# Kernel optimization log

Hardware: AMD Instinct MI355X
Metric: run time of the kernel (lower is better)

## Reference

```python
import jax, jax.numpy as jnp
import numpy as np

B, L, D, H, K = 4, 4096, 1024, 16, 256

def setup_inputs() -> dict:
    key = jax.random.key(0)
    ks = jax.random.split(key, 11)
    s = 0.02
    return {
        "x": jax.random.normal(ks[0], (B, L, D), jnp.float32),
        "Wq": jax.random.normal(ks[1], (D, D), jnp.float32) * s,
        "bq": jax.random.normal(ks[2], (D,), jnp.float32) * s,
        "Wk": jax.random.normal(ks[3], (D, D), jnp.float32) * s,
        "bk": jax.random.normal(ks[4], (D,), jnp.float32) * s,
        "Wv": jax.random.normal(ks[5], (D, D), jnp.float32) * s,
        "bv": jax.random.normal(ks[6], (D,), jnp.float32) * s,
        "E": jax.random.normal(ks[7], (L, K), jnp.float32),
        "F": jax.random.normal(ks[8], (L, K), jnp.float32),
        "Wo": jax.random.normal(ks[9], (D, D), jnp.float32) * s,
        "bo": jax.random.normal(ks[10], (D,), jnp.float32) * s,
        "n_heads": H,
    }

def reference(x, Wq, bq, Wk, bk, Wv, bv, E, F, Wo, bo, n_heads):
    Bc, Lc, Dc = x.shape
    hd = Dc // n_heads
    scale = hd ** -0.5
    # QKV projections (torch Linear: x @ W.T + b; here W stored as [in,out])
    q = (x @ Wq + bq).reshape(Bc, Lc, n_heads, hd)  # blhd
    k = (x @ Wk + bk).reshape(Bc, Lc, n_heads, hd)
    v = (x @ Wv + bv).reshape(Bc, Lc, n_heads, hd)
    # Low-rank projection of K/V sequence dim: L -> K
    kE = jnp.einsum('blhd,lk->bhkd', k, E[:Lc])
    vF = jnp.einsum('blhd,lk->bhkd', v, F[:Lc])
    # Attention over compressed dim k
    qk = jnp.einsum('blhd,bhkd->bhlk', q, kE) * scale
    attn = jax.nn.softmax(qk, axis=-1)
    out = jnp.einsum('bhlk,bhkd->blhd', attn, vF).reshape(Bc, Lc, Dc)
    return out @ Wo + bo
```

## Files before the change

kernel.cpp:

```cpp
#include <hip/hip_runtime.h>

typedef _Float16 half_t;
typedef __attribute__((ext_vector_type(8))) _Float16 f16x8;
typedef __attribute__((ext_vector_type(4))) _Float16 f16x4;
typedef __attribute__((ext_vector_type(4))) float f32x4;
typedef __attribute__((ext_vector_type(4))) float float4v;

__device__ __forceinline__ void gload_lds16(const void* g, void* l) {
  __builtin_amdgcn_global_load_lds(
      (const __attribute__((address_space(1))) void*)g,
      (__attribute__((address_space(3))) void*)l, 16, 0, 0);
}

template<int OUTMODE>
__global__ __launch_bounds__(512, 2)
void gemm_big(const half_t* __restrict__ A, const half_t* __restrict__ Bt,
              void* __restrict__ Cv, const float* __restrict__ bias, float alpha)
{
  __shared__ __attribute__((aligned(16))) char lds[131072];
  const int tid = threadIdx.x, w = tid >> 6, lane = tid & 63;
  const int wr = w >> 2, wc = w & 3;
  const int g = lane >> 4, cc = lane & 15;
  const int m0 = blockIdx.x * 256, n0 = blockIdx.y * 256;

  const int srow2 = tid >> 2, sslot = tid & 3;
  const int swslot = sslot ^ ((srow2 >> 1) & 3);
  const int swr = (g ^ ((cc >> 1) & 3)) << 4;

  const f32x4 zero = {0.f, 0.f, 0.f, 0.f};
  f32x4 acc[8][4];
#pragma unroll
  for (int i = 0; i < 8; ++i)
#pragma unroll
    for (int j = 0; j < 4; ++j) acc[i][j] = zero;

  auto STAGE_HALF = [&](int ktile, int hh, char* sb) {
    const int kk = hh >> 1, isB = hh & 1;
    const half_t* src = isB ? Bt : A;
    const int base_row = isB ? n0 : m0;
    const long rowoff = (long)(base_row + srow2) * 1024 + ktile * 64 + kk * 32 + swslot * 8;
    char* d = sb + isB * 32768 + kk * 16384;
    gload_lds16(src + rowoff,          d + tid * 16);
    gload_lds16(src + rowoff + 131072, d + 8192 + tid * 16);
  };

  {
    char* b0 = lds;
    STAGE_HALF(0, 0, b0); STAGE_HALF(0, 1, b0);
    STAGE_HALF(0, 2, b0); STAGE_HALF(0, 3, b0);
  }
  asm volatile("s_waitcnt vmcnt(4)" ::: "memory");
  __builtin_amdgcn_s_barrier();

#pragma unroll 1
  for (int n = 0; n < 16; ++n) {
    const char* rb = lds + ((n & 1) << 16);
    char* sb = lds + (((n + 1) & 1) << 16);
    f16x8 bf[4];
#pragma unroll
    for (int ph = 0; ph < 4; ++ph) {
      const int kk = ph >> 1, fh = ph & 1;
      f16x8 af[4];
      const char* Ah = rb + kk * 16384;
#pragma unroll
      for (int mf = 0; mf < 4; ++mf)
        af[mf] = *(const f16x8*)(Ah + (wr * 128 + fh * 64 + mf * 16 + cc) * 64 + swr);
      if (fh == 0) {
        const char* Bh = rb + 32768 + kk * 16384;
#pragma unroll
        for (int nf = 0; nf < 4; ++nf)
          bf[nf] = *(const f16x8*)(Bh + (wc * 64 + nf * 16 + cc) * 64 + swr);
      }
      if (n < 15) STAGE_HALF(n + 1, ph, sb);
      __builtin_amdgcn_sched_barrier(0);
      __builtin_amdgcn_s_barrier();
      asm volatile("s_waitcnt lgkmcnt(0)" ::: "memory");
      __builtin_amdgcn_sched_barrier(0);
      __builtin_amdgcn_s_setprio(1);
#pragma unroll
      for (int mf = 0; mf < 4; ++mf)
#pragma unroll
        for (int nf = 0; nf < 4; ++nf)
          acc[fh * 4 + mf][nf] =
              __builtin_amdgcn_mfma_f32_16x16x32_f16(af[mf], bf[nf], acc[fh * 4 + mf][nf], 0, 0, 0);
      __builtin_amdgcn_s_setprio(0);
      __builtin_amdgcn_sched_barrier(0);
      if (ph == 1) {
        if (n < 15) { asm volatile("s_waitcnt vmcnt(4)" ::: "memory"); }
        else        { asm volatile("s_waitcnt vmcnt(0)" ::: "memory"); }
      } else if (ph == 3) {
        if (n < 15) { asm volatile("s_waitcnt vmcnt(4)" ::: "memory"); }
      }
      __builtin_amdgcn_s_barrier();
    }
  }

#pragma unroll
  for (int mf = 0; mf < 8; ++mf)
#pragma unroll
    for (int nf = 0; nf < 4; ++nf)
#pragma unroll
      for (int r = 0; r < 4; ++r) {
        const int row = m0 + wr * 128 + mf * 16 + g * 4 + r;
        const int col = n0 + wc * 64 + nf * 16 + cc;
        float v = (acc[mf][nf][r] + bias[col]) * alpha;
        if (OUTMODE == 0) {
          ((float*)Cv)[(long)row * 1024 + col] = v;
        } else {
          const int bb = row >> 12, l = row & 4095, h = col >> 6, d = col & 63;
          ((half_t*)Cv)[(((long)(bb * 16 + h) * 4096 + l) << 6) + d] = (half_t)v;
        }
      }
}

template<int SK>
__global__ __launch_bounds__(256, 2)
void gemm_xef(const half_t* __restrict__ A, const half_t* __restrict__ Bt,
              float* __restrict__ Cv, int lda, int ldb, long sB, long sC)
{
  __shared__ __attribute__((aligned(16))) half_t As[128 * 32];
  __shared__ __attribute__((aligned(16))) half_t Bs[128 * 32];

  const int tid = threadIdx.x, w = tid >> 6, lane = tid & 63;
  const int wr = w >> 1, wc = w & 1;
  const int z = blockIdx.z / SK, ks = blockIdx.z % SK;
  const half_t* Ab = A;
  const half_t* Bb = Bt + (long)z * sB;
  const int m0 = blockIdx.x * 128, n0 = blockIdx.y * 128;
  const int g = lane >> 4, cc = lane & 15;
  const int srow = lane >> 2, scol = (lane & 3) * 8;

  const f32x4 zero = {0.f, 0.f, 0.f, 0.f};
  f32x4 acc[4][4];
#pragma unroll
  for (int i = 0; i < 4; ++i)
#pragma unroll
    for (int j = 0; j < 4; ++j) acc[i][j] = zero;

  const int kchunk = 4096 / SK;
  for (int kt = ks * kchunk; kt < (ks + 1) * kchunk; kt += 32) {
#pragma unroll
    for (int j = 0; j < 2; ++j) {
      const int bi = w * 2 + j;
      gload_lds16(Ab + (long)(m0 + bi * 16 + srow) * lda + kt + scol, &As[bi * 512]);
      gload_lds16(Bb + (long)(n0 + bi * 16 + srow) * ldb + kt + scol, &Bs[bi * 512]);
    }
    __syncthreads();

    f16x8 af[4], bf[4];
#pragma unroll
    for (int i = 0; i < 4; ++i)
      af[i] = *(const f16x8*)&As[(wr * 64 + i * 16 + cc) * 32 + g * 8];
#pragma unroll
    for (int j = 0; j < 4; ++j)
      bf[j] = *(const f16x8*)&Bs[(wc * 64 + j * 16 + cc) * 32 + g * 8];
#pragma unroll
    for (int i = 0; i < 4; ++i)
#pragma unroll
      for (int j = 0; j < 4; ++j)
        acc[i][j] = __builtin_amdgcn_mfma_f32_16x16x32_f16(af[i], bf[j], acc[i][j], 0, 0, 0);
    __syncthreads();
  }

  const int nb = gridDim.z / SK;
#pragma unroll
  for (int i = 0; i < 4; ++i)
#pragma unroll
    for (int j = 0; j < 4; ++j)
#pragma unroll
      for (int r = 0; r < 4; ++r) {
        const int row = m0 + wr * 64 + i * 16 + g * 4 + r;
        const int col = n0 + wc * 64 + j * 16 + cc;
        Cv[((long)ks * nb + z) * sC + (long)row * 1024 + col] = acc[i][j][r];
      }
}

__global__ __launch_bounds__(256, 2)
void gemm_kevf(const half_t* __restrict__ xEF, const half_t* __restrict__ Wkt,
               const half_t* __restrict__ Wvt, half_t* __restrict__ kEb,
               half_t* __restrict__ vFtb, const float* __restrict__ bk,
               const float* __restrict__ bv, const float* __restrict__ sEF)
{
  __shared__ __attribute__((aligned(16))) half_t As[64 * 32];
  __shared__ __attribute__((aligned(16))) half_t Bs[64 * 32];
  const int tid = threadIdx.x, w = tid >> 6, lane = tid & 63;
  const int wr = w >> 1, wc = w & 1;
  const int g = lane >> 4, cc = lane & 15;
  const int srow = lane >> 2, scol = (lane & 3) * 8;

  const int bid = blockIdx.x;
  const int role = bid >> 8, lb = bid & 255;
  const half_t *Ap, *Bp;
  int m0, n0, z;
  if (role == 0) {
    m0 = (lb & 3) * 64; n0 = ((lb >> 2) & 15) * 64; z = lb >> 6;
    Ap = xEF + (long)z * 524288;  Bp = Wkt;
  } else {
    m0 = (lb & 15) * 64; n0 = ((lb >> 4) & 3) * 64; z = lb >> 6;
    Ap = Wvt;  Bp = xEF + (long)z * 524288 + 262144;
  }

  const f32x4 zero = {0.f, 0.f, 0.f, 0.f};
  f32x4 acc[2][2];
#pragma unroll
  for (int i = 0; i < 2; ++i)
#pragma unroll
    for (int j = 0; j < 2; ++j) acc[i][j] = zero;

  for (int kt = 0; kt < 1024; kt += 32) {
    gload_lds16(Ap + (long)(m0 + w * 16 + srow) * 1024 + kt + scol, &As[w * 512]);
    gload_lds16(Bp + (long)(n0 + w * 16 + srow) * 1024 + kt + scol, &Bs[w * 512]);
    __syncthreads();
    f16x8 af[2], bf[2];
#pragma unroll
    for (int i = 0; i < 2; ++i)
      af[i] = *(const f16x8*)&As[(wr * 32 + i * 16 + cc) * 32 + g * 8];
#pragma unroll
    for (int j = 0; j < 2; ++j)
      bf[j] = *(const f16x8*)&Bs[(wc * 32 + j * 16 + cc) * 32 + g * 8];
#pragma unroll
    for (int i = 0; i < 2; ++i)
#pragma unroll
      for (int j = 0; j < 2; ++j)
        acc[i][j] = __builtin_amdgcn_mfma_f32_16x16x32_f16(af[i], bf[j], acc[i][j], 0, 0, 0);
    __syncthreads();
  }

#pragma unroll
  for (int i = 0; i < 2; ++i)
#pragma unroll
    for (int j = 0; j < 2; ++j)
#pragma unroll
      for (int r = 0; r < 4; ++r) {
        const int row = m0 + wr * 32 + i * 16 + g * 4 + r;
        const int col = n0 + wc * 32 + j * 16 + cc;
        float v = acc[i][j][r];
        if (role == 0) {
          v += sEF[row] * bk[col];
          kEb[(long)z * 262144 + (long)(col >> 6) * 16384 + (long)row * 64 + (col & 63)]
              = (half_t)v;
        } else {
          v += bv[row] * sEF[256 + col];
          vFtb[(long)z * 262144 + (long)row * 256 + col] = (half_t)v;
        }
      }
}

__global__ __launch_bounds__(512, 2)
void attn_fused(const half_t* __restrict__ qhb, const half_t* __restrict__ kEh,
                const half_t* __restrict__ vFt, half_t* __restrict__ outp, int L)
{
  __shared__ __attribute__((aligned(16))) half_t Ks[256 * 64];
  __shared__ __attribute__((aligned(16))) half_t Vs[64 * 256];
  const int tid = threadIdx.x, w = tid >> 6, lane = tid & 63;
  const int g = lane >> 4, c = lane & 15;
  const int l0 = blockIdx.x * 256, h = blockIdx.y, b = blockIdx.z;

  const half_t* keh = kEh + (long)(b * 16 + h) * 16384;
  const half_t* vfh = vFt + (long)b * 262144 + (long)h * 16384;
  const half_t* qpan = qhb + ((long)(b * 16 + h) * 4096 + l0) * 64;
  half_t* ob = outp + ((long)b * L + l0 + w * 32) * 1024 + h * 64;

#pragma unroll
  for (int i = 0; i < 4; ++i) {
    const int row = i * 64 + (tid >> 3), slot = tid & 7;
    gload_lds16(keh + row * 64 + ((slot ^ (row & 7)) << 3),
                (char*)Ks + i * 8192 + tid * 16);
  }
#pragma unroll
  for (int i = 0; i < 4; ++i) {
    const int row = i * 16 + (tid >> 5), slot = tid & 31;
    gload_lds16(vfh + row * 256 + ((slot ^ (row & 7)) << 3),
                (char*)Vs + i * 8192 + tid * 16);
  }

  f16x8 qf[2][2];
#pragma unroll
  for (int fi = 0; fi < 2; ++fi)
#pragma unroll
    for (int ks = 0; ks < 2; ++ks)
      qf[fi][ks] = *(const f16x8*)(qpan + (w * 32 + fi * 16 + c) * 64 + ks * 32 + g * 8);

  __syncthreads();

  const f32x4 zero = {0.f, 0.f, 0.f, 0.f};
  f32x4 o[2][4];
#pragma unroll
  for (int fi = 0; fi < 2; ++fi)
#pragma unroll
    for (int fd = 0; fd < 4; ++fd) o[fi][fd] = zero;
  float mrun[2] = {-3.0e38f, -3.0e38f};
  float lrun[2] = {0.f, 0.f};

  for (int ch = 0; ch < 4; ++ch) {
    f32x4 s[2][4];
#pragma unroll
    for (int fi = 0; fi < 2; ++fi)
#pragma unroll
      for (int fj = 0; fj < 4; ++fj) s[fi][fj] = zero;
#pragma unroll
    for (int fj = 0; fj < 4; ++fj) {
      const int krow = ch * 64 + fj * 16 + c;
      const char* kb = (const char*)Ks + krow * 128;
      f16x8 k0 = *(const f16x8*)(kb + ((g ^ (c & 7)) << 4));
      f16x8 k1 = *(const f16x8*)(kb + (((4 + g) ^ (c & 7)) << 4));
#pragma unroll
      for (int fi = 0; fi < 2; ++fi) {
        s[fi][fj] = __builtin_amdgcn_mfma_f32_16x16x32_f16(k0, qf[fi][0], s[fi][fj], 0, 0, 0);
        s[fi][fj] = __builtin_amdgcn_mfma_f32_16x16x32_f16(k1, qf[fi][1], s[fi][fj], 0, 0, 0);
      }
    }

    f16x4 p[2][4];
#pragma unroll
    for (int fi = 0; fi < 2; ++fi) {
      float cm = -3.0e38f;
#pragma unroll
      for (int fj = 0; fj < 4; ++fj)
#pragma unroll
        for (int r = 0; r < 4; ++r) cm = fmaxf(cm, s[fi][fj][r]);
      cm = fmaxf(cm, __shfl_xor(cm, 16));
      cm = fmaxf(cm, __shfl_xor(cm, 32));
      const float mref = mrun[fi];
      const bool keep = __all(cm - mref <= 8.0f);
      const float mnew = keep ? mref : fmaxf(mref, cm);
      float csum = 0.f;
#pragma unroll
      for (int fj = 0; fj < 4; ++fj) {
        f16x4 fr;
#pragma unroll
        for (int r = 0; r < 4; ++r) {
          float e = __expf(s[fi][fj][r] - mnew);
          fr[r] = (half_t)e; csum += e;
        }
        p[fi][fj] = fr;
      }
      csum += __shfl_xor(csum, 16);
      csum += __shfl_xor(csum, 32);
      if (keep) {
        lrun[fi] += csum;
      } else {
        const float sc = __expf(mref - mnew);
        lrun[fi] = lrun[fi] * sc + csum;
        mrun[fi] = mnew;
#pragma unroll
        for (int fd = 0; fd < 4; ++fd)
#pragma unroll
          for (int r = 0; r < 4; ++r) o[fi][fd][r] *= sc;
      }
    }

#pragma unroll
    for (int kc = 0; kc < 4; ++kc) {
      const int s16 = ch * 8 + kc * 2 + (g >> 1);
      f16x4 va[4];
#pragma unroll
      for (int fd = 0; fd < 4; ++fd) {
        const int drow = fd * 16 + c;
        va[fd] = *(const f16x4*)((const char*)Vs + drow * 512 +
                                 ((s16 ^ (c & 7)) << 4) + (g & 1) * 8);
      }
#pragma unroll
      for (int fi = 0; fi < 2; ++fi)
#pragma unroll
        for (int fd = 0; fd < 4; ++fd)
          o[fi][fd] = __builtin_amdgcn_mfma_f32_16x16x16f16(va[fd], p[fi][kc], o[fi][fd], 0, 0, 0);
    }
  }

#pragma unroll
  for (int fi = 0; fi < 2; ++fi) {
    const float inv = 1.0f / lrun[fi];
#pragma unroll
    for (int fd = 0; fd < 4; ++fd) {
      f16x4 st;
#pragma unroll
      for (int r = 0; r < 4; ++r) st[r] = (half_t)(o[fi][fd][r] * inv);
      *(f16x4*)(ob + (long)(fi * 16 + c) * 1024 + fd * 16 + g * 4) = st;
    }
  }
}

__global__ __launch_bounds__(256, 4)
void prepass(const float* __restrict__ x, half_t* __restrict__ xhf,
             half_t* __restrict__ xT,
             const float* __restrict__ E, const float* __restrict__ F,
             half_t* __restrict__ EFt, float* __restrict__ sEF,
             const float* __restrict__ Wq, const float* __restrict__ Wk,
             const float* __restrict__ Wv, const float* __restrict__ Wo,
             half_t* __restrict__ Wqt, half_t* __restrict__ Wkt,
             half_t* __restrict__ Wvt, half_t* __restrict__ Wot)
{
  __shared__ float t[64][65];
  __shared__ float ps[4][64];
  const int tx = threadIdx.x, ty = threadIdx.y;
  const int id = blockIdx.x;

  if (id < 4096) {
    const int bx = id & 15, by = (id >> 4) & 63, bz = id >> 10;
    const int d0 = bx * 64, l0 = by * 64;
    const float* ip = x + ((long)bz * 4096 + l0) * 1024 + d0;
    half_t* oh = xhf + ((long)bz * 4096 + l0) * 1024 + d0;
#pragma unroll
    for (int j = 0; j < 16; ++j) {
      const int row = ty + 4 * j;
      float v = ip[(long)row * 1024 + tx];
      t[row][tx] = v;
      oh[(long)row * 1024 + tx] = (half_t)v;
    }
    __syncthreads();
    half_t* ot = xT + ((long)bz * 1024 + d0) * 4096 + l0;
#pragma unroll
    for (int j = 0; j < 16; ++j) {
      const int drow = ty + 4 * j;
      ot[(long)drow * 4096 + tx] = (half_t)t[tx][drow];
    }
  } else if (id < 4608) {
    const int id2 = id - 4096;
    const int bx = id2 & 3, by = (id2 >> 2) & 63, zz = id2 >> 8;
    const float* in = zz ? F : E;
    half_t* oT = EFt + (long)zz * 1048576;
    float* sm = sEF + zz * 256;
    const int k0 = bx * 64, l0 = by * 64;
    float p = 0.f;
#pragma unroll
    for (int j = 0; j < 16; ++j) {
      const int row = ty + 4 * j;
      float v = in[(long)(l0 + row) * 256 + k0 + tx];
      t[row][tx] = v; p += v;
    }
    ps[ty][tx] = p;
    __syncthreads();
    if (ty == 0) {
      float a = ps[0][tx] + ps[1][tx] + ps[2][tx] + ps[3][tx];
      atomicAdd(&sm[k0 + tx], a);
    }
#pragma unroll
    for (int j = 0; j < 16; ++j) {
      const int krow = ty + 4 * j;
      oT[(long)(k0 + krow) * 4096 + l0 + tx] = (half_t)t[tx][krow];
    }
  } else {
    const int id3 = id - 4608;
    const int bx = id3 & 15, by = (id3 >> 4) & 15, zz = id3 >> 8;
    const float* in = (zz == 0) ? Wq : (zz == 1) ? Wk : (zz == 2) ? Wv : Wo;
    half_t* out = (zz == 0) ? Wqt : (zz == 1) ? Wkt : (zz == 2) ? Wvt : Wot;
    const int c0 = bx * 64, r0 = by * 64;
#pragma unroll
    for (int j = 0; j < 16; ++j) {
      const int row = ty + 4 * j;
      t[row][tx] = in[(long)(r0 + row) * 1024 + c0 + tx];
    }
    __syncthreads();
#pragma unroll
    for (int j = 0; j < 16; ++j) {
      const int crow = ty + 4 * j;
      out[(long)(c0 + crow) * 1024 + r0 + tx] = (half_t)t[tx][crow];
    }
  }
}

__global__ void reduce4_f16(const float* __restrict__ in, half_t* __restrict__ out) {
  long i = ((long)blockIdx.x * 256 + threadIdx.x) * 4;
  float4v a = *(const float4v*)(in + i);
#pragma unroll
  for (int ks = 1; ks < 4; ++ks) {
    float4v t = *(const float4v*)(in + (long)ks * 2097152 + i);
    a.x += t.x; a.y += t.y; a.z += t.z; a.w += t.w;
  }
  f16x4 o;
  o[0] = (half_t)a.x; o[1] = (half_t)a.y; o[2] = (half_t)a.z; o[3] = (half_t)a.w;
  *(f16x4*)(out + i) = o;
}

extern "C" void kernel_launch(void* const* d_in, const int* in_sizes, int n_in,
                              void* d_out, int out_size, void* d_ws, size_t ws_size,
                              hipStream_t stream)
{
  const float* x  = (const float*)d_in[0];
  const float* Wq = (const float*)d_in[1];
  const float* bq = (const float*)d_in[2];
  const float* Wk = (const float*)d_in[3];
  const float* bk = (const float*)d_in[4];
  const float* Wv = (const float*)d_in[5];
  const float* bv = (const float*)d_in[6];
  const float* E  = (const float*)d_in[7];
  const float* F  = (const float*)d_in[8];
  const float* Wo = (const float*)d_in[9];
  const float* bo = (const float*)d_in[10];
  float* out = (float*)d_out;

  char* ws = (char*)d_ws;
  half_t* xhf  = (half_t*)(ws);
  half_t* xT   = (half_t*)(ws + 33554432);
  half_t* qhf  = (half_t*)(ws + 67108864);
  half_t* Wqt  = (half_t*)(ws + 100663296);
  half_t* Wkt  = Wqt + 1048576;
  half_t* Wvt  = Wkt + 1048576;
  half_t* Wot  = Wvt + 1048576;
  half_t* EFt  = (half_t*)(ws + 109051904);
  half_t* xEF  = (half_t*)(ws + 113246208);
  half_t* kEb  = (half_t*)(ws + 117440512);
  half_t* vFtb = (half_t*)(ws + 119537664);
  float*  sEF  = (float*)(ws + 121634816);
  half_t* outp = xhf;
  float*  xEFf = (float*)d_out;

  hipMemsetAsync(sEF, 0, 2048, stream);
  prepass<<<dim3(5632), dim3(64, 4), 0, stream>>>(
      x, xhf, xT, E, F, EFt, sEF, Wq, Wk, Wv, Wo, Wqt, Wkt, Wvt, Wot);

  gemm_xef<4><<<dim3(4, 8, 16), 256, 0, stream>>>(
      EFt, xT, xEFf, 4096, 4096, 4194304, 524288);
  reduce4_f16<<<2048, 256, 0, stream>>>(xEFf, xEF);

  gemm_big<2><<<dim3(64, 4), 512, 0, stream>>>(xhf, Wqt, qhf, bq, 0.125f);
  gemm_kevf<<<dim3(512), 256, 0, stream>>>(xEF, Wkt, Wvt, kEb, vFtb, bk, bv, sEF);
  attn_fused<<<dim3(16, 16, 4), 512, 0, stream>>>(qhf, kEb, vFtb, outp, 4096);
  gemm_big<0><<<dim3(64, 4), 512, 0, stream>>>(outp, Wot, (void*)out, bo, 1.0f);
  (void)bq; (void)in_sizes; (void)n_in; (void)out_size; (void)ws_size;
}
```

Baseline: 213.8 us.

## Store attention output head-major, process two tiles per block, use exp2 softmax

The attention kernel now writes its output in a head-major [b,h,l,64] layout, giving contiguous 128-byte rows instead of strided writes into the [b,l,1024] matrix. The output-projection GEMM gains an address mode that gathers A tiles from that layout. Each attention block now handles two 256-row query tiles, so the K/V staging into LDS is amortised over more work with half as many blocks. Softmax switches to exp2f, with log2(e) folded into the Q scale and the rescale threshold adjusted to match.

```diff
diff --git a/kernel.cpp b/kernel.cpp
--- a/kernel.cpp
+++ b/kernel.cpp
@@ -12,7 +12,7 @@
       (__attribute__((address_space(3))) void*)l, 16, 0, 0);
 }
 
-template<int OUTMODE>
+template<int OUTMODE, int AMODE>
 __global__ __launch_bounds__(512, 2)
 void gemm_big(const half_t* __restrict__ A, const half_t* __restrict__ Bt,
               void* __restrict__ Cv, const float* __restrict__ bias, float alpha)
@@ -36,12 +36,22 @@
 
   auto STAGE_HALF = [&](int ktile, int hh, char* sb) {
     const int kk = hh >> 1, isB = hh & 1;
-    const half_t* src = isB ? Bt : A;
-    const int base_row = isB ? n0 : m0;
-    const long rowoff = (long)(base_row + srow2) * 1024 + ktile * 64 + kk * 32 + swslot * 8;
     char* d = sb + isB * 32768 + kk * 16384;
-    gload_lds16(src + rowoff,          d + tid * 16);
-    gload_lds16(src + rowoff + 131072, d + 8192 + tid * 16);
+    if (!isB && AMODE == 1) {
+      const int r0 = m0 + srow2, r1 = r0 + 128;
+      const long a0 = (((long)((r0 >> 12) * 16 + ktile) * 4096 + (r0 & 4095)) << 6)
+                      + kk * 32 + swslot * 8;
+      const long a1 = (((long)((r1 >> 12) * 16 + ktile) * 4096 + (r1 & 4095)) << 6)
+                      + kk * 32 + swslot * 8;
+      gload_lds16(A + a0, d + tid * 16);
+      gload_lds16(A + a1, d + 8192 + tid * 16);
+    } else {
+      const half_t* src = isB ? Bt : A;
+      const int base_row = isB ? n0 : m0;
+      const long rowoff = (long)(base_row + srow2) * 1024 + ktile * 64 + kk * 32 + swslot * 8;
+      gload_lds16(src + rowoff,          d + tid * 16);
+      gload_lds16(src + rowoff + 131072, d + 8192 + tid * 16);
+    }
   };
 
   {
@@ -254,12 +264,10 @@
   __shared__ __attribute__((aligned(16))) half_t Vs[64 * 256];
   const int tid = threadIdx.x, w = tid >> 6, lane = tid & 63;
   const int g = lane >> 4, c = lane & 15;
-  const int l0 = blockIdx.x * 256, h = blockIdx.y, b = blockIdx.z;
+  const int l0 = blockIdx.x * 512, h = blockIdx.y, b = blockIdx.z;
 
   const half_t* keh = kEh + (long)(b * 16 + h) * 16384;
   const half_t* vfh = vFt + (long)b * 262144 + (long)h * 16384;
-  const half_t* qpan = qhb + ((long)(b * 16 + h) * 4096 + l0) * 64;
-  half_t* ob = outp + ((long)b * L + l0 + w * 32) * 1024 + h * 64;
 
 #pragma unroll
   for (int i = 0; i < 4; ++i) {
@@ -273,110 +281,117 @@
     gload_lds16(vfh + row * 256 + ((slot ^ (row & 7)) << 3),
                 (char*)Vs + i * 8192 + tid * 16);
   }
-
-  f16x8 qf[2][2];
-#pragma unroll
-  for (int fi = 0; fi < 2; ++fi)
-#pragma unroll
-    for (int ks = 0; ks < 2; ++ks)
-      qf[fi][ks] = *(const f16x8*)(qpan + (w * 32 + fi * 16 + c) * 64 + ks * 32 + g * 8);
-
   __syncthreads();
 
   const f32x4 zero = {0.f, 0.f, 0.f, 0.f};
-  f32x4 o[2][4];
-#pragma unroll
-  for (int fi = 0; fi < 2; ++fi)
-#pragma unroll
-    for (int fd = 0; fd < 4; ++fd) o[fi][fd] = zero;
-  float mrun[2] = {-3.0e38f, -3.0e38f};
-  float lrun[2] = {0.f, 0.f};
-
-  for (int ch = 0; ch < 4; ++ch) {
-    f32x4 s[2][4];
+
+#pragma unroll 1
+  for (int tt = 0; tt < 2; ++tt) {
+    const long lbase = (long)(b * 16 + h) * 4096 + l0 + tt * 256;
+    const half_t* qpan = qhb + lbase * 64;
+    half_t* ob = outp + (lbase + w * 32) * 64;
+
+    f16x8 qf[2][2];
 #pragma unroll
     for (int fi = 0; fi < 2; ++fi)
 #pragma unroll
-      for (int fj = 0; fj < 4; ++fj) s[fi][fj] = zero;
-#pragma unroll
-    for (int fj = 0; fj < 4; ++fj) {
-      const int krow = ch * 64 + fj * 16 + c;
-      const char* kb = (const char*)Ks + krow * 128;
-      f16x8 k0 = *(const f16x8*)(kb + ((g ^ (c & 7)) << 4));
-      f16x8 k1 = *(const f16x8*)(kb + (((4 + g) ^ (c & 7)) << 4));
+      for (int ks = 0; ks < 2; ++ks)
+        qf[fi][ks] = *(const f16x8*)(qpan + (w * 32 + fi * 16 + c) * 64 + ks * 32 + g * 8);
+
+    f32x4 o[2][4];
+#pragma unroll
+    for (int fi = 0; fi < 2; ++fi)
+#pragma unroll
+      for (int fd = 0; fd < 4; ++fd) o[fi][fd] = zero;
+    float mrun[2] = {-3.0e38f, -3.0e38f};
+    float lrun[2] = {0.f, 0.f};
+
+    for (int ch = 0; ch < 4; ++ch) {
+      f32x4 s[2][4];
+#pragma unroll
+      for (int fi = 0; fi < 2; ++fi)
+#pragma unroll
+        for (int fj = 0; fj < 4; ++fj) s[fi][fj] = zero;
+#pragma unroll
+      for (int fj = 0; fj < 4; ++fj) {
+        const int krow = ch * 64 + fj * 16 + c;
+        const char* kb = (const char*)Ks + krow * 128;
+        f16x8 k0 = *(const f16x8*)(kb + ((g ^ (c & 7)) << 4));
+        f16x8 k1 = *(const f16x8*)(kb + (((4 + g) ^ (c & 7)) << 4));
+#pragma unroll
+        for (int fi = 0; fi < 2; ++fi) {
+          s[fi][fj] = __builtin_amdgcn_mfma_f32_16x16x32_f16(k0, qf[fi][0], s[fi][fj], 0, 0, 0);
+          s[fi][fj] = __builtin_amdgcn_mfma_f32_16x16x32_f16(k1, qf[fi][1], s[fi][fj], 0, 0, 0);
+        }
+      }
+
+      f16x4 p[2][4];
 #pragma unroll
       for (int fi = 0; fi < 2; ++fi) {
-        s[fi][fj] = __builtin_amdgcn_mfma_f32_16x16x32_f16(k0, qf[fi][0], s[fi][fj], 0, 0, 0);
-        s[fi][fj] = __builtin_amdgcn_mfma_f32_16x16x32_f16(k1, qf[fi][1], s[fi][fj], 0, 0, 0);
-      }
-    }
-
-    f16x4 p[2][4];
+        float cm = -3.0e38f;
+#pragma unroll
+        for (int fj = 0; fj < 4; ++fj)
+#pragma unroll
+          for (int r = 0; r < 4; ++r) cm = fmaxf(cm, s[fi][fj][r]);
+        cm = fmaxf(cm, __shfl_xor(cm, 16));
+        cm = fmaxf(cm, __shfl_xor(cm, 32));
+        const float mref = mrun[fi];
+        const bool keep = __all(cm - mref <= 11.5442495f);
+        const float mnew = keep ? mref : fmaxf(mref, cm);
+        float csum = 0.f;
+#pragma unroll
+        for (int fj = 0; fj < 4; ++fj) {
+          f16x4 fr;
+#pragma unroll
+          for (int r = 0; r < 4; ++r) {
+            float e = exp2f(s[fi][fj][r] - mnew);
+            fr[r] = (half_t)e; csum += e;
+          }
+          p[fi][fj] = fr;
+        }
+        csum += __shfl_xor(csum, 16);
+        csum += __shfl_xor(csum, 32);
+        if (keep) {
+          lrun[fi] += csum;
+        } else {
+          const float sc = exp2f(mref - mnew);
+          lrun[fi] = lrun[fi] * sc + csum;
+          mrun[fi] = mnew;
+#pragma unroll
+          for (int fd = 0; fd < 4; ++fd)
+#pragma unroll
+            for (int r = 0; r < 4; ++r) o[fi][fd][r] *= sc;
+        }
+      }
+
+#pragma unroll
+      for (int kc = 0; kc < 4; ++kc) {
+        const int s16 = ch * 8 + kc * 2 + (g >> 1);
+        f16x4 va[4];
+#pragma unroll
+        for (int fd = 0; fd < 4; ++fd) {
+          const int drow = fd * 16 + c;
+          va[fd] = *(const f16x4*)((const char*)Vs + drow * 512 +
+                                   ((s16 ^ (c & 7)) << 4) + (g & 1) * 8);
+        }
+#pragma unroll
+        for (int fi = 0; fi < 2; ++fi)
+#pragma unroll
+          for (int fd = 0; fd < 4; ++fd)
+            o[fi][fd] = __builtin_amdgcn_mfma_f32_16x16x16f16(va[fd], p[fi][kc], o[fi][fd], 0, 0, 0);
+      }
+    }
+
 #pragma unroll
     for (int fi = 0; fi < 2; ++fi) {
-      float cm = -3.0e38f;
-#pragma unroll
-      for (int fj = 0; fj < 4; ++fj)
-#pragma unroll
-        for (int r = 0; r < 4; ++r) cm = fmaxf(cm, s[fi][fj][r]);
-      cm = fmaxf(cm, __shfl_xor(cm, 16));
-      cm = fmaxf(cm, __shfl_xor(cm, 32));
-      const float mref = mrun[fi];
-      const bool keep = __all(cm - mref <= 8.0f);
-      const float mnew = keep ? mref : fmaxf(mref, cm);
-      float csum = 0.f;
-#pragma unroll
-      for (int fj = 0; fj < 4; ++fj) {
-        f16x4 fr;
-#pragma unroll
-        for (int r = 0; r < 4; ++r) {
-          float e = __expf(s[fi][fj][r] - mnew);
-          fr[r] = (half_t)e; csum += e;
-        }
-        p[fi][fj] = fr;
-      }
-      csum += __shfl_xor(csum, 16);
-      csum += __shfl_xor(csum, 32);
-      if (keep) {
-        lrun[fi] += csum;
-      } else {
-        const float sc = __expf(mref - mnew);
-        lrun[fi] = lrun[fi] * sc + csum;
-        mrun[fi] = mnew;
-#pragma unroll
-        for (int fd = 0; fd < 4; ++fd)
-#pragma unroll
-          for (int r = 0; r < 4; ++r) o[fi][fd][r] *= sc;
-      }
-    }
-
-#pragma unroll
-    for (int kc = 0; kc < 4; ++kc) {
-      const int s16 = ch * 8 + kc * 2 + (g >> 1);
-      f16x4 va[4];
+      const float inv = 1.0f / lrun[fi];
 #pragma unroll
       for (int fd = 0; fd < 4; ++fd) {
-        const int drow = fd * 16 + c;
-        va[fd] = *(const f16x4*)((const char*)Vs + drow * 512 +
-                                 ((s16 ^ (c & 7)) << 4) + (g & 1) * 8);
-      }
-#pragma unroll
-      for (int fi = 0; fi < 2; ++fi)
-#pragma unroll
-        for (int fd = 0; fd < 4; ++fd)
-          o[fi][fd] = __builtin_amdgcn_mfma_f32_16x16x16f16(va[fd], p[fi][kc], o[fi][fd], 0, 0, 0);
-    }
-  }
-
-#pragma unroll
-  for (int fi = 0; fi < 2; ++fi) {
-    const float inv = 1.0f / lrun[fi];
-#pragma unroll
-    for (int fd = 0; fd < 4; ++fd) {
-      f16x4 st;
-#pragma unroll
-      for (int r = 0; r < 4; ++r) st[r] = (half_t)(o[fi][fd][r] * inv);
-      *(f16x4*)(ob + (long)(fi * 16 + c) * 1024 + fd * 16 + g * 4) = st;
+        f16x4 st;
+#pragma unroll
+        for (int r = 0; r < 4; ++r) st[r] = (half_t)(o[fi][fd][r] * inv);
+        *(f16x4*)(ob + (long)(fi * 16 + c) * 64 + fd * 16 + g * 4) = st;
+      }
     }
   }
 }
@@ -514,9 +529,9 @@
       EFt, xT, xEFf, 4096, 4096, 4194304, 524288);
   reduce4_f16<<<2048, 256, 0, stream>>>(xEFf, xEF);
 
-  gemm_big<2><<<dim3(64, 4), 512, 0, stream>>>(xhf, Wqt, qhf, bq, 0.125f);
+  gemm_big<2,0><<<dim3(64, 4), 512, 0, stream>>>(xhf, Wqt, qhf, bq, 0.1803368801f);
   gemm_kevf<<<dim3(512), 256, 0, stream>>>(xEF, Wkt, Wvt, kEb, vFtb, bk, bv, sEF);
-  attn_fused<<<dim3(16, 16, 4), 512, 0, stream>>>(qhf, kEb, vFtb, outp, 4096);
-  gemm_big<0><<<dim3(64, 4), 512, 0, stream>>>(outp, Wot, (void*)out, bo, 1.0f);
-  (void)bq; (void)in_sizes; (void)n_in; (void)out_size; (void)ws_size;
-}
+  attn_fused<<<dim3(8, 16, 4), 512, 0, stream>>>(qhf, kEb, vFtb, outp, 4096);
+  gemm_big<0,1><<<dim3(64, 4), 512, 0, stream>>>(outp, Wot, (void*)out, bo, 1.0f);
+  (void)in_sizes; (void)n_in; (void)out_size; (void)ws_size;
+}
```

After: 213.1 us (median of 2 runs). Within noise of the previous version (-0.3%).
